# Optimization experiments

Hardware: AMD Instinct MI355X
Metric: run time of the kernel (lower is better)

## Reference

```python
import jax, jax.numpy as jnp
import numpy as np

DIM = 384
HEADS = 6
N_TOKEN = 2240
HIDDEN = int(DIM * 4.0)
EPS = 1e-5


def layernorm(x, g, b):
    mu = jnp.mean(x, axis=-1, keepdims=True)
    var = jnp.mean(jnp.square(x - mu), axis=-1, keepdims=True)
    return (x - mu) * jax.lax.rsqrt(var + EPS) * g + b


def setup_inputs() -> dict:
    key = jax.random.key(0)
    ks = jax.random.split(key, 10)
    B, N, C = 2, 2240, DIM
    s = 0.02
    return {
        "x": jax.random.normal(ks[0], (B, N, C), dtype=jnp.float32),
        "encoder_pos": jax.random.normal(ks[1], (1, N_TOKEN, C), dtype=jnp.float32) * s,
        "ln1_g": jnp.ones((C,), jnp.float32),
        "ln1_b": jnp.zeros((C,), jnp.float32),
        "w_qkv": jax.random.normal(ks[2], (3 * C, C), dtype=jnp.float32) * s,  # torch Linear [out,in], no bias
        "w_proj": jax.random.normal(ks[3], (C, C), dtype=jnp.float32) * s,
        "b_proj": jnp.zeros((C,), jnp.float32),
        "ln2_g": jnp.ones((C,), jnp.float32),
        "ln2_b": jnp.zeros((C,), jnp.float32),
        "w_fc1": jax.random.normal(ks[4], (HIDDEN, C), dtype=jnp.float32) * s,
        "b_fc1": jnp.zeros((HIDDEN,), jnp.float32),
        "w_fc2": jax.random.normal(ks[5], (C, HIDDEN), dtype=jnp.float32) * s,
        "b_fc2": jnp.zeros((C,), jnp.float32),
    }


def reference(x, encoder_pos, ln1_g, ln1_b, w_qkv, w_proj, b_proj, ln2_g, ln2_b, w_fc1, b_fc1, w_fc2, b_fc2):
    B, N, C = x.shape
    H = HEADS
    hd = C // H
    scale = hd ** -0.5

    # positional embedding: each of the n_token rows repeated N//n_token times (contiguously)
    rep = N // encoder_pos.shape[1]
    pos = jnp.repeat(encoder_pos, rep, axis=1)  # [1, N, C]
    x = x + pos

    # attention
    h = layernorm(x, ln1_g, ln1_b)
    qkv = h @ w_qkv.T  # [B, N, 3C]
    qkv = qkv.reshape(B, N, 3, H, hd).transpose(2, 0, 3, 1, 4)  # [3, B, H, N, hd]
    q, k, v = qkv[0], qkv[1], qkv[2]
    attn = jax.nn.softmax(jnp.einsum("bhqd,bhkd->bhqk", q, k) * scale, axis=-1)  # [B, H, N, N]
    o = jnp.einsum("bhqk,bhkd->bhqd", attn, v).transpose(0, 2, 1, 3).reshape(B, N, C)
    o = o @ w_proj.T + b_proj
    x = x + o

    # MLP
    h = layernorm(x, ln2_g, ln2_b)
    h = jax.nn.gelu(h @ w_fc1.T + b_fc1, approximate=False)
    h = h @ w_fc2.T + b_fc2
    x = x + h
    return (x, attn)
```

## Files before the change

### kernel.cpp

```cpp
#include <hip/hip_runtime.h>
#include <math.h>

typedef unsigned short u16;
typedef unsigned int   u32;
typedef __attribute__((ext_vector_type(8))) short short8;
typedef __attribute__((ext_vector_type(4))) float floatx4;

#define MFMA16(a,b,c) __builtin_amdgcn_mfma_f32_16x16x32_bf16((a),(b),(c),0,0,0)

constexpr int BB  = 2;
constexpr int NT  = 2240;
constexpr int CD  = 384;
constexpr int NH  = 6;
constexpr int HD  = 64;
constexpr int HID = 1536;
constexpr int M   = BB * NT;
constexpr int CS  = 5;
constexpr int CTILES = NT / 64 / CS;
constexpr float SCALE = 0.125f;

__device__ inline u16 f2bf(float f) {
  u32 u = __float_as_uint(f);
  u = (u + 0x7fffu + ((u >> 16) & 1u)) >> 16;
  return (u16)u;
}
__device__ inline float bf2f(u16 b) { return __uint_as_float(((u32)b) << 16); }

__device__ inline void gload16(const u16* g, u16* l) {
  __builtin_amdgcn_global_load_lds(
      (const __attribute__((address_space(1))) u32*)g,
      (__attribute__((address_space(3))) u32*)l, 16, 0, 0);
}

__device__ inline uint4 sum5_bf(uint4 a0, uint4 a1, uint4 a2, uint4 a3, uint4 a4) {
  union U { uint4 v; u16 h[8]; };
  U u0, u1, u2, u3, u4, o;
  u0.v = a0; u1.v = a1; u2.v = a2; u3.v = a3; u4.v = a4;
  #pragma unroll
  for (int e = 0; e < 8; ++e) {
    float f = bf2f(u0.h[e]) + bf2f(u1.h[e]) + bf2f(u2.h[e]) + bf2f(u3.h[e]) + bf2f(u4.h[e]);
    o.h[e] = f2bf(f);
  }
  return o.v;
}

constexpr int NQ = 3 * CD * CD, NP = CD * CD, N1 = HID * CD, N2 = CD * HID;
constexpr int CVT_BLOCKS = (NQ + NP + N1 + N2) / 512;

__global__ __launch_bounds__(128) void ln_cvt_kernel(
    const float* __restrict__ xin, const float* __restrict__ pos,
    const float* __restrict__ g, const float* __restrict__ bta,
    float* __restrict__ x1out, u16* __restrict__ hout,
    const float* __restrict__ s0, u16* __restrict__ d0,
    const float* __restrict__ s1, u16* __restrict__ d1,
    const float* __restrict__ s2, u16* __restrict__ d2,
    const float* __restrict__ s3, u16* __restrict__ d3) {
  int t = threadIdx.x;
  if (blockIdx.x >= M) {
    int i = ((blockIdx.x - M) * 128 + t) * 4;
    const float* s; u16* d; int base;
    if (i < NQ)                { s = s0; d = d0; base = 0; }
    else if (i < NQ + NP)      { s = s1; d = d1; base = NQ; }
    else if (i < NQ + NP + N1) { s = s2; d = d2; base = NQ + NP; }
    else                       { s = s3; d = d3; base = NQ + NP + N1; }
    int j = i - base;
    float4 v = *(const float4*)(s + j);
    ushort4 o; o.x = f2bf(v.x); o.y = f2bf(v.y); o.z = f2bf(v.z); o.w = f2bf(v.w);
    *(ushort4*)(d + j) = o;
    return;
  }
  int row = blockIdx.x;
  int n = row % NT;
  const float* xr = xin + (size_t)row * CD;
  float v[3], s1v = 0.f, s2v = 0.f;
  #pragma unroll
  for (int j = 0; j < 3; ++j) {
    int c = t + j * 128;
    float x = xr[c] + pos[(size_t)n * CD + c];
    v[j] = x; s1v += x; s2v += x * x;
  }
  #pragma unroll
  for (int off = 32; off; off >>= 1) { s1v += __shfl_down(s1v, off); s2v += __shfl_down(s2v, off); }
  __shared__ float rbuf[4];
  __shared__ float stats[2];
  int lane = t & 63, wid = t >> 6;
  if (lane == 0) { rbuf[wid] = s1v; rbuf[2 + wid] = s2v; }
  __syncthreads();
  if (t == 0) {
    float a = rbuf[0] + rbuf[1], b2 = rbuf[2] + rbuf[3];
    float mu = a / CD;
    float var = b2 / CD - mu * mu;
    stats[0] = mu; stats[1] = rsqrtf(var + 1e-5f);
  }
  __syncthreads();
  float mu = stats[0], rs = stats[1];
  #pragma unroll
  for (int j = 0; j < 3; ++j) {
    int c = t + j * 128;
    float h = (v[j] - mu) * rs * g[c] + bta[c];
    hout[(size_t)row * CD + c] = f2bf(h);
    x1out[(size_t)row * CD + c] = v[j];
  }
}

template <int EPI, int AMODE>
__global__ __launch_bounds__(256) void gemm_bt(
    const u16* __restrict__ A, const float* __restrict__ Af,
    const u16* __restrict__ Wt, int K,
    const float* __restrict__ bias, const float* __restrict__ res,
    const float* __restrict__ lng, const float* __restrict__ lnb,
    float* __restrict__ outf, u16* __restrict__ outb,
    u16* __restrict__ qout, u16* __restrict__ kout, u16* __restrict__ vtout) {
  __shared__ __align__(16) u16 As[64][64];
  __shared__ __align__(16) u16 Bs[64][64];
  __shared__ float mu_s[64], rs_s[64];
  int m0 = blockIdx.y * 64, n0 = blockIdx.x * 64;
  int t = threadIdx.x;
  int lane = t & 63, w = t >> 6, wm = w & 1, wn = w >> 1;
  int quad = lane >> 4, c16 = lane & 15;
  int lrow = t >> 2, lseg = t & 3;
  int l8 = lane >> 3;
  int colsel = ((lane & 7) ^ l8) * 8;
  int r7 = c16 & 7;

  const u16* gbsrc = Wt + (size_t)(n0 + w * 16 + l8) * K + colsel;
  u16* ldsB = &Bs[w * 16][0];
  const u16* gasrc = nullptr; u16* ldsA = nullptr;
  if constexpr (AMODE == 0) {
    gasrc = A + (size_t)(m0 + w * 16 + l8) * K + colsel;
    ldsA = &As[w * 16][0];
  }

  if constexpr (AMODE == 2) {
    const float* xr = Af + (size_t)(m0 + lrow) * CD + lseg * 96;
    float s1 = 0.f, s2 = 0.f;
    #pragma unroll
    for (int j2 = 0; j2 < 24; ++j2) {
      float4 v = *(const float4*)(xr + j2 * 4);
      s1 += v.x + v.y + v.z + v.w;
      s2 += v.x * v.x + v.y * v.y + v.z * v.z + v.w * v.w;
    }
    s1 += __shfl_xor(s1, 1); s2 += __shfl_xor(s2, 1);
    s1 += __shfl_xor(s1, 2); s2 += __shfl_xor(s2, 2);
    if (lseg == 0) {
      float mu = s1 / CD, var = s2 / CD - mu * mu;
      mu_s[lrow] = mu; rs_s[lrow] = rsqrtf(var + 1e-5f);
    }
  }

  constexpr int SL = (AMODE == 1) ? 5 : 1;
  const u16* ga[SL];
  uint4 av0[SL], av1[SL];
  float4 lf0, lf1, lf2, lf3;
  if constexpr (AMODE == 1) {
    #pragma unroll
    for (int s = 0; s < SL; ++s) {
      ga[s] = A + (size_t)s * M * CD + (size_t)(m0 + lrow) * CD + lseg * 8;
      av0[s] = *(const uint4*)(ga[s]);
      av1[s] = *(const uint4*)(ga[s] + 32);
    }
  } else if constexpr (AMODE == 2) {
    const float* ar = Af + (size_t)(m0 + lrow) * CD + lseg * 8;
    lf0 = *(const float4*)(ar);      lf1 = *(const float4*)(ar + 4);
    lf2 = *(const float4*)(ar + 32); lf3 = *(const float4*)(ar + 36);
  }

  floatx4 acc[2][2] = {};
  for (int k0 = 0; k0 < K; k0 += 64) {
    __syncthreads();
    #pragma unroll
    for (int j = 0; j < 2; ++j) {
      gload16(gbsrc + (size_t)j * 8 * K + k0, ldsB + j * 512);
      if constexpr (AMODE == 0)
        gload16(gasrc + (size_t)j * 8 * K + k0, ldsA + j * 512);
    }
    if constexpr (AMODE == 1) {
      uint4 wa0 = sum5_bf(av0[0], av0[1], av0[2], av0[3], av0[4]);
      uint4 wa1 = sum5_bf(av1[0], av1[1], av1[2], av1[3], av1[4]);
      *(uint4*)&As[lrow][(lseg ^ (lrow & 7)) * 8] = wa0;
      *(uint4*)&As[lrow][((4 + lseg) ^ (lrow & 7)) * 8] = wa1;
    } else if constexpr (AMODE == 2) {
      float mu = mu_s[lrow], rs = rs_s[lrow];
      union { uint4 v; u16 h[8]; } pk;
      int cb = k0 + lseg * 8;
      float4 g0 = *(const float4*)(lng + cb), g1 = *(const float4*)(lng + cb + 4);
      float4 b0 = *(const float4*)(lnb + cb), b1 = *(const float4*)(lnb + cb + 4);
      pk.h[0] = f2bf((lf0.x - mu) * rs * g0.x + b0.x);
      pk.h[1] = f2bf((lf0.y - mu) * rs * g0.y + b0.y);
      pk.h[2] = f2bf((lf0.z - mu) * rs * g0.z + b0.z);
      pk.h[3] = f2bf((lf0.w - mu) * rs * g0.w + b0.w);
      pk.h[4] = f2bf((lf1.x - mu) * rs * g1.x + b1.x);
      pk.h[5] = f2bf((lf1.y - mu) * rs * g1.y + b1.y);
      pk.h[6] = f2bf((lf1.z - mu) * rs * g1.z + b1.z);
      pk.h[7] = f2bf((lf1.w - mu) * rs * g1.w + b1.w);
      *(uint4*)&As[lrow][(lseg ^ (lrow & 7)) * 8] = pk.v;
      int cb2 = cb + 32;
      float4 g2 = *(const float4*)(lng + cb2), g3 = *(const float4*)(lng + cb2 + 4);
      float4 b2 = *(const float4*)(lnb + cb2), b3 = *(const float4*)(lnb + cb2 + 4);
      pk.h[0] = f2bf((lf2.x - mu) * rs * g2.x + b2.x);
      pk.h[1] = f2bf((lf2.y - mu) * rs * g2.y + b2.y);
      pk.h[2] = f2bf((lf2.z - mu) * rs * g2.z + b2.z);
      pk.h[3] = f2bf((lf2.w - mu) * rs * g2.w + b2.w);
      pk.h[4] = f2bf((lf3.x - mu) * rs * g3.x + b3.x);
      pk.h[5] = f2bf((lf3.y - mu) * rs * g3.y + b3.y);
      pk.h[6] = f2bf((lf3.z - mu) * rs * g3.z + b3.z);
      pk.h[7] = f2bf((lf3.w - mu) * rs * g3.w + b3.w);
      *(uint4*)&As[lrow][((4 + lseg) ^ (lrow & 7)) * 8] = pk.v;
    }
    __syncthreads();
    if (k0 + 64 < K) {
      if constexpr (AMODE == 1) {
        #pragma unroll
        for (int s = 0; s < SL; ++s) {
          av0[s] = *(const uint4*)(ga[s] + k0 + 64);
          av1[s] = *(const uint4*)(ga[s] + k0 + 96);
        }
      } else if constexpr (AMODE == 2) {
        const float* ar = Af + (size_t)(m0 + lrow) * CD + k0 + 64 + lseg * 8;
        lf0 = *(const float4*)(ar);      lf1 = *(const float4*)(ar + 4);
        lf2 = *(const float4*)(ar + 32); lf3 = *(const float4*)(ar + 36);
      }
    }
    #pragma unroll
    for (int ks = 0; ks < 2; ++ks) {
      int cswz = ((ks * 4 + quad) ^ r7) * 8;
      short8 af[2], bf[2];
      #pragma unroll
      for (int mt = 0; mt < 2; ++mt) af[mt] = *(const short8*)&As[wm * 32 + mt * 16 + c16][cswz];
      #pragma unroll
      for (int nt = 0; nt < 2; ++nt) bf[nt] = *(const short8*)&Bs[wn * 32 + nt * 16 + c16][cswz];
      #pragma unroll
      for (int mt = 0; mt < 2; ++mt)
        #pragma unroll
        for (int nt = 0; nt < 2; ++nt)
          acc[mt][nt] = MFMA16(af[mt], bf[nt], acc[mt][nt]);
    }
  }
  if constexpr (EPI == 0) {
    int s = n0 / 384;
    int hh = (n0 % 384) / 64;
    int b_ = m0 / NT, nn0 = m0 % NT;
    __syncthreads();
    #pragma unroll
    for (int mt = 0; mt < 2; ++mt)
      #pragma unroll
      for (int nt = 0; nt < 2; ++nt)
        #pragma unroll
        for (int r = 0; r < 4; ++r) {
          int m_l = wm * 32 + mt * 16 + quad * 4 + r;
          int d_l = wn * 32 + nt * 16 + c16;
          u16 bv = f2bf(acc[mt][nt][r]);
          if (s < 2) As[m_l][d_l ^ ((m_l & 7) << 3)] = bv;
          else       As[d_l][m_l ^ ((d_l & 7) << 3)] = bv;
        }
    __syncthreads();
    int row = t >> 2, q2 = (t & 3) * 2;
    uint4 va = *(const uint4*)&As[row][(q2 ^ (row & 7)) * 8];
    uint4 vb = *(const uint4*)&As[row][((q2 + 1) ^ (row & 7)) * 8];
    int cs0 = (t & 3) * 16;
    u16* dst;
    if (s == 0)      dst = qout  + ((size_t)(b_ * NH + hh) * NT + nn0 + row) * HD + cs0;
    else if (s == 1) dst = kout  + ((size_t)(b_ * NH + hh) * NT + nn0 + row) * HD + cs0;
    else             dst = vtout + ((size_t)(b_ * NH + hh) * HD + row) * NT + nn0 + cs0;
    *(uint4*)dst = va;
    *(uint4*)(dst + 8) = vb;
  } else {
    #pragma unroll
    for (int mt = 0; mt < 2; ++mt) {
      #pragma unroll
      for (int nt = 0; nt < 2; ++nt) {
        int rg0 = m0 + wm * 32 + mt * 16 + quad * 4;
        int cg = n0 + wn * 32 + nt * 16 + c16;
        #pragma unroll
        for (int r = 0; r < 4; ++r) {
          float v = acc[mt][nt][r];
          int m = rg0 + r;
          if constexpr (EPI == 2) {
            v += bias[cg];
            v = 0.5f * v * (1.0f + erff(v * 0.70710678118f));
            outb[(size_t)m * HID + cg] = f2bf(v);
          } else {
            outf[(size_t)m * CD + cg] = v + bias[cg] + res[(size_t)m * CD + cg];
          }
        }
      }
    }
  }
}

__global__ __launch_bounds__(256) void attn_pass1(
    const u16* __restrict__ qb, const u16* __restrict__ kb, float* __restrict__ ml) {
  __shared__ __align__(16) u16 Ks[64][72];
  int bh = blockIdx.y, chunk = blockIdx.z;
  int q0 = blockIdx.x * 64;
  int t = threadIdx.x, w = t >> 6, lane = t & 63, quad = lane >> 4, c16 = lane & 15;
  int lrow = t >> 2, lseg = t & 3;

  const u16* qp = qb + ((size_t)bh * NT + q0 + w * 16 + c16) * HD;
  short8 qf0 = *(const short8*)(qp + quad * 8);
  short8 qf1 = *(const short8*)(qp + 32 + quad * 8);
  const u16* kbase = kb + (size_t)bh * NT * HD;

  float m_i = -1e30f, l_i = 0.f;

  const u16* kg = kbase + (size_t)(chunk * CTILES * 64 + lrow) * HD + lseg * 8;
  uint4 kv0 = *(const uint4*)kg;
  uint4 kv1 = *(const uint4*)(kg + 32);

  for (int ct = 0; ct < CTILES; ++ct) {
    __syncthreads();
    *(uint4*)&Ks[lrow][lseg * 8] = kv0;
    *(uint4*)&Ks[lrow][32 + lseg * 8] = kv1;
    __syncthreads();
    if (ct + 1 < CTILES) {
      const u16* kn = kbase + (size_t)((chunk * CTILES + ct + 1) * 64 + lrow) * HD + lseg * 8;
      kv0 = *(const uint4*)kn;
      kv1 = *(const uint4*)(kn + 32);
    }
    floatx4 s_acc[4] = {};
    #pragma unroll
    for (int nt = 0; nt < 4; ++nt) {
      const u16* kp = &Ks[nt * 16 + c16][quad * 8];
      s_acc[nt] = MFMA16(*(const short8*)(kp), qf0, s_acc[nt]);
      s_acc[nt] = MFMA16(*(const short8*)(kp + 32), qf1, s_acc[nt]);
    }
    float rm = -1e30f;
    #pragma unroll
    for (int nt = 0; nt < 4; ++nt)
      #pragma unroll
      for (int r = 0; r < 4; ++r) rm = fmaxf(rm, s_acc[nt][r]);
    rm *= SCALE;
    rm = fmaxf(rm, __shfl_xor(rm, 16));
    rm = fmaxf(rm, __shfl_xor(rm, 32));
    float nm = fmaxf(m_i, rm);
    float ps = 0.f;
    #pragma unroll
    for (int nt = 0; nt < 4; ++nt)
      #pragma unroll
      for (int r = 0; r < 4; ++r) ps += __expf(s_acc[nt][r] * SCALE - nm);
    ps += __shfl_xor(ps, 16);
    ps += __shfl_xor(ps, 32);
    l_i = l_i * __expf(m_i - nm) + ps;
    m_i = nm;
  }
  if (quad == 0) {
    int row = q0 + w * 16 + c16;
    float* p = ml + ((size_t)(bh * NT + row) * CS + chunk) * 2;
    p[0] = m_i; p[1] = l_i;
  }
}

__global__ __launch_bounds__(256) void attn_pass2(
    const u16* __restrict__ qb, const u16* __restrict__ kb, const u16* __restrict__ vtb,
    const float* __restrict__ ml, float* __restrict__ attn_out, u16* __restrict__ o_part) {
  __shared__ __align__(16) u16 Ks[64][72];
  __shared__ __align__(16) u16 Vs[64][72];
  __shared__ __align__(16) u16 Plds[4][16][72];
  __shared__ float mfin[64], rlfin[64];
  int bh = blockIdx.y, chunk = blockIdx.z;
  int b = bh / NH, hh = bh % NH;
  int q0 = blockIdx.x * 64;
  int t = threadIdx.x, w = t >> 6, lane = t & 63, quad = lane >> 4, c16 = lane & 15;
  int lrow = t >> 2, lseg = t & 3;

  const u16* kbase = kb + (size_t)bh * NT * HD;
  const u16* vbase = vtb + (size_t)bh * HD * NT;

  int col00 = chunk * CTILES * 64;
  const u16* kg = kbase + (size_t)(col00 + lrow) * HD + lseg * 8;
  const u16* vg = vbase + (size_t)lrow * NT + col00 + lseg * 8;
  uint4 kv0 = *(const uint4*)kg;
  uint4 kv1 = *(const uint4*)(kg + 32);
  uint4 vv0 = *(const uint4*)vg;
  uint4 vv1 = *(const uint4*)(vg + 32);

  if (t < 64) {
    const float* p = ml + (size_t)(bh * NT + q0 + t) * CS * 2;
    float mm = -1e30f;
    #pragma unroll
    for (int c = 0; c < CS; ++c) mm = fmaxf(mm, p[c * 2]);
    float ll = 0.f;
    #pragma unroll
    for (int c = 0; c < CS; ++c) ll += p[c * 2 + 1] * __expf(p[c * 2] - mm);
    mfin[t] = mm; rlfin[t] = 1.0f / ll;
  }
  __syncthreads();
  float m_i[4], rl[4];
  #pragma unroll
  for (int r = 0; r < 4; ++r) {
    int rr = w * 16 + quad * 4 + r;
    m_i[r] = mfin[rr]; rl[r] = rlfin[rr];
  }

  const u16* qp = qb + ((size_t)bh * NT + q0 + w * 16 + c16) * HD;
  short8 qf0 = *(const short8*)(qp + quad * 8);
  short8 qf1 = *(const short8*)(qp + 32 + quad * 8);

  floatx4 o_acc[4] = {};
  float* attn_bh = attn_out + (size_t)bh * NT * NT;
  for (int ct = 0; ct < CTILES; ++ct) {
    int col0 = (chunk * CTILES + ct) * 64;
    __syncthreads();
    *(uint4*)&Ks[lrow][lseg * 8] = kv0;
    *(uint4*)&Ks[lrow][32 + lseg * 8] = kv1;
    *(uint4*)&Vs[lrow][lseg * 8] = vv0;
    *(uint4*)&Vs[lrow][32 + lseg * 8] = vv1;
    __syncthreads();
    if (ct + 1 < CTILES) {
      int coln = col0 + 64;
      const u16* kn = kbase + (size_t)(coln + lrow) * HD + lseg * 8;
      const u16* vn = vbase + (size_t)lrow * NT + coln + lseg * 8;
      kv0 = *(const uint4*)kn;
      kv1 = *(const uint4*)(kn + 32);
      vv0 = *(const uint4*)vn;
      vv1 = *(const uint4*)(vn + 32);
    }
    floatx4 s_acc[4] = {};
    #pragma unroll
    for (int nt = 0; nt < 4; ++nt) {
      const u16* kp = &Ks[nt * 16 + c16][quad * 8];
      s_acc[nt] = MFMA16(qf0, *(const short8*)(kp), s_acc[nt]);
      s_acc[nt] = MFMA16(qf1, *(const short8*)(kp + 32), s_acc[nt]);
    }
    #pragma unroll
    for (int nt = 0; nt < 4; ++nt) {
      #pragma unroll
      for (int r = 0; r < 4; ++r) {
        float p = __expf(s_acc[nt][r] * SCALE - m_i[r]) * rl[r];
        __builtin_nontemporal_store(
            p, &attn_bh[(size_t)(q0 + w * 16 + quad * 4 + r) * NT + col0 + nt * 16 + c16]);
        Plds[w][quad * 4 + r][nt * 16 + c16] = f2bf(p);
      }
    }
    #pragma unroll
    for (int ks = 0; ks < 2; ++ks) {
      short8 pa = *(const short8*)&Plds[w][c16][ks * 32 + quad * 8];
      #pragma unroll
      for (int dt = 0; dt < 4; ++dt) {
        short8 vb = *(const short8*)&Vs[dt * 16 + c16][ks * 32 + quad * 8];
        o_acc[dt] = MFMA16(pa, vb, o_acc[dt]);
      }
    }
  }
  #pragma unroll
  for (int dt = 0; dt < 4; ++dt) {
    #pragma unroll
    for (int r = 0; r < 4; ++r) {
      int m = b * NT + q0 + w * 16 + quad * 4 + r;
      int cc = hh * 64 + dt * 16 + c16;
      o_part[((size_t)chunk * M + m) * CD + cc] = f2bf(o_acc[dt][r]);
    }
  }
}

extern "C" void kernel_launch(void* const* d_in, const int* in_sizes, int n_in,
                              void* d_out, int out_size, void* d_ws, size_t ws_size,
                              hipStream_t stream) {
  const float* x      = (const float*)d_in[0];
  const float* pos    = (const float*)d_in[1];
  const float* ln1_g  = (const float*)d_in[2];
  const float* ln1_b  = (const float*)d_in[3];
  const float* w_qkv  = (const float*)d_in[4];
  const float* w_proj = (const float*)d_in[5];
  const float* b_proj = (const float*)d_in[6];
  const float* ln2_g  = (const float*)d_in[7];
  const float* ln2_b  = (const float*)d_in[8];
  const float* w_fc1  = (const float*)d_in[9];
  const float* b_fc1  = (const float*)d_in[10];
  const float* w_fc2  = (const float*)d_in[11];
  const float* b_fc2  = (const float*)d_in[12];

  float* out      = (float*)d_out;
  float* attn_out = out + (size_t)M * CD;

  char* ws = (char*)d_ws;
  size_t o = 0;
  auto carve = [&](size_t bytes) { char* p = ws + o; o += bytes; return p; };
  float* x1    = (float*)carve((size_t)M * CD * 4);
  u16* h1      = (u16*)carve((size_t)M * CD * 2);
  u16* wqkv_b  = (u16*)carve((size_t)3 * CD * CD * 2);
  u16* wproj_b = (u16*)carve((size_t)CD * CD * 2);
  u16* wfc1_b  = (u16*)carve((size_t)HID * CD * 2);
  u16* wfc2_b  = (u16*)carve((size_t)CD * HID * 2);
  u16* q_bf    = (u16*)carve((size_t)BB * NH * NT * HD * 2);
  u16* k_bf    = (u16*)carve((size_t)BB * NH * NT * HD * 2);
  u16* vt_bf   = (u16*)carve((size_t)BB * NH * NT * HD * 2);
  float* x2    = (float*)carve((size_t)M * CD * 4);
  u16* g_bf    = (u16*)carve((size_t)M * HID * 2);
  float* ml    = (float*)carve((size_t)NH * BB * NT * CS * 2 * 4);
  u16* o_part  = (u16*)carve((size_t)CS * M * CD * 2);
  (void)ws_size; (void)in_sizes; (void)n_in; (void)out_size;

  ln_cvt_kernel<<<M + CVT_BLOCKS, 128, 0, stream>>>(
      x, pos, ln1_g, ln1_b, x1, h1,
      w_qkv, wqkv_b, w_proj, wproj_b, w_fc1, wfc1_b, w_fc2, wfc2_b);

  gemm_bt<0, 0><<<dim3((3 * CD) / 64, M / 64), 256, 0, stream>>>(
      h1, nullptr, wqkv_b, CD, nullptr, nullptr, nullptr, nullptr,
      nullptr, nullptr, q_bf, k_bf, vt_bf);

  attn_pass1<<<dim3(NT / 64, BB * NH, CS), 256, 0, stream>>>(q_bf, k_bf, ml);
  attn_pass2<<<dim3(NT / 64, BB * NH, CS), 256, 0, stream>>>(q_bf, k_bf, vt_bf, ml, attn_out, o_part);

  gemm_bt<3, 1><<<dim3(CD / 64, M / 64), 256, 0, stream>>>(
      o_part, nullptr, wproj_b, CD, b_proj, x1, nullptr, nullptr,
      x2, nullptr, nullptr, nullptr, nullptr);

  gemm_bt<2, 2><<<dim3(HID / 64, M / 64), 256, 0, stream>>>(
      nullptr, x2, wfc1_b, CD, b_fc1, nullptr, ln2_g, ln2_b,
      nullptr, g_bf, nullptr, nullptr, nullptr);

  gemm_bt<3, 0><<<dim3(CD / 64, M / 64), 256, 0, stream>>>(
      g_bf, nullptr, wfc2_b, HID, b_fc2, x2, nullptr, nullptr,
      out, nullptr, nullptr, nullptr, nullptr);
}
```

Before: 432.8 us.

## Replace direct global-to-LDS loads with register-staged prefetch and padded LDS tiles

```diff
diff --git a/kernel.cpp b/kernel.cpp
--- a/kernel.cpp
+++ b/kernel.cpp
@@ -25,12 +25,6 @@
   return (u16)u;
 }
 __device__ inline float bf2f(u16 b) { return __uint_as_float(((u32)b) << 16); }
-
-__device__ inline void gload16(const u16* g, u16* l) {
-  __builtin_amdgcn_global_load_lds(
-      (const __attribute__((address_space(1))) u32*)g,
-      (__attribute__((address_space(3))) u32*)l, 16, 0, 0);
-}
 
 __device__ inline uint4 sum5_bf(uint4 a0, uint4 a1, uint4 a2, uint4 a3, uint4 a4) {
   union U { uint4 v; u16 h[8]; };
@@ -111,25 +105,14 @@
     const float* __restrict__ lng, const float* __restrict__ lnb,
     float* __restrict__ outf, u16* __restrict__ outb,
     u16* __restrict__ qout, u16* __restrict__ kout, u16* __restrict__ vtout) {
-  __shared__ __align__(16) u16 As[64][64];
-  __shared__ __align__(16) u16 Bs[64][64];
+  __shared__ __align__(16) u16 As[64][72];
+  __shared__ __align__(16) u16 Bs[64][72];
   __shared__ float mu_s[64], rs_s[64];
   int m0 = blockIdx.y * 64, n0 = blockIdx.x * 64;
   int t = threadIdx.x;
   int lane = t & 63, w = t >> 6, wm = w & 1, wn = w >> 1;
   int quad = lane >> 4, c16 = lane & 15;
   int lrow = t >> 2, lseg = t & 3;
-  int l8 = lane >> 3;
-  int colsel = ((lane & 7) ^ l8) * 8;
-  int r7 = c16 & 7;
-
-  const u16* gbsrc = Wt + (size_t)(n0 + w * 16 + l8) * K + colsel;
-  u16* ldsB = &Bs[w * 16][0];
-  const u16* gasrc = nullptr; u16* ldsA = nullptr;
-  if constexpr (AMODE == 0) {
-    gasrc = A + (size_t)(m0 + w * 16 + l8) * K + colsel;
-    ldsA = &As[w * 16][0];
-  }
 
   if constexpr (AMODE == 2) {
     const float* xr = Af + (size_t)(m0 + lrow) * CD + lseg * 96;
@@ -155,7 +138,7 @@
   if constexpr (AMODE == 1) {
     #pragma unroll
     for (int s = 0; s < SL; ++s) {
-      ga[s] = A + (size_t)s * M * CD + (size_t)(m0 + lrow) * CD + lseg * 8;
+      ga[s] = A + (size_t)s * M * CD + (size_t)(m0 + lrow) * K + lseg * 8;
       av0[s] = *(const uint4*)(ga[s]);
       av1[s] = *(const uint4*)(ga[s] + 32);
     }
@@ -163,22 +146,23 @@
     const float* ar = Af + (size_t)(m0 + lrow) * CD + lseg * 8;
     lf0 = *(const float4*)(ar);      lf1 = *(const float4*)(ar + 4);
     lf2 = *(const float4*)(ar + 32); lf3 = *(const float4*)(ar + 36);
-  }
+  } else {
+    ga[0] = A + (size_t)(m0 + lrow) * K + lseg * 8;
+    av0[0] = *(const uint4*)(ga[0]);
+    av1[0] = *(const uint4*)(ga[0] + 32);
+  }
+  const u16* gb = Wt + (size_t)(n0 + lrow) * K + lseg * 8;
+  uint4 bv0 = *(const uint4*)(gb);
+  uint4 bv1 = *(const uint4*)(gb + 32);
 
   floatx4 acc[2][2] = {};
   for (int k0 = 0; k0 < K; k0 += 64) {
     __syncthreads();
-    #pragma unroll
-    for (int j = 0; j < 2; ++j) {
-      gload16(gbsrc + (size_t)j * 8 * K + k0, ldsB + j * 512);
-      if constexpr (AMODE == 0)
-        gload16(gasrc + (size_t)j * 8 * K + k0, ldsA + j * 512);
-    }
     if constexpr (AMODE == 1) {
       uint4 wa0 = sum5_bf(av0[0], av0[1], av0[2], av0[3], av0[4]);
       uint4 wa1 = sum5_bf(av1[0], av1[1], av1[2], av1[3], av1[4]);
-      *(uint4*)&As[lrow][(lseg ^ (lrow & 7)) * 8] = wa0;
-      *(uint4*)&As[lrow][((4 + lseg) ^ (lrow & 7)) * 8] = wa1;
+      *(uint4*)&As[lrow][lseg * 8] = wa0;
+      *(uint4*)&As[lrow][32 + lseg * 8] = wa1;
     } else if constexpr (AMODE == 2) {
       float mu = mu_s[lrow], rs = rs_s[lrow];
       union { uint4 v; u16 h[8]; } pk;
@@ -193,7 +177,7 @@
       pk.h[5] = f2bf((lf1.y - mu) * rs * g1.y + b1.y);
       pk.h[6] = f2bf((lf1.z - mu) * rs * g1.z + b1.z);
       pk.h[7] = f2bf((lf1.w - mu) * rs * g1.w + b1.w);
-      *(uint4*)&As[lrow][(lseg ^ (lrow & 7)) * 8] = pk.v;
+      *(uint4*)&As[lrow][lseg * 8] = pk.v;
       int cb2 = cb + 32;
       float4 g2 = *(const float4*)(lng + cb2), g3 = *(const float4*)(lng + cb2 + 4);
       float4 b2 = *(const float4*)(lnb + cb2), b3 = *(const float4*)(lnb + cb2 + 4);
@@ -205,8 +189,13 @@
       pk.h[5] = f2bf((lf3.y - mu) * rs * g3.y + b3.y);
       pk.h[6] = f2bf((lf3.z - mu) * rs * g3.z + b3.z);
       pk.h[7] = f2bf((lf3.w - mu) * rs * g3.w + b3.w);
-      *(uint4*)&As[lrow][((4 + lseg) ^ (lrow & 7)) * 8] = pk.v;
-    }
+      *(uint4*)&As[lrow][32 + lseg * 8] = pk.v;
+    } else {
+      *(uint4*)&As[lrow][lseg * 8] = av0[0];
+      *(uint4*)&As[lrow][32 + lseg * 8] = av1[0];
+    }
+    *(uint4*)&Bs[lrow][lseg * 8] = bv0;
+    *(uint4*)&Bs[lrow][32 + lseg * 8] = bv1;
     __syncthreads();
     if (k0 + 64 < K) {
       if constexpr (AMODE == 1) {
@@ -219,16 +208,20 @@
         const float* ar = Af + (size_t)(m0 + lrow) * CD + k0 + 64 + lseg * 8;
         lf0 = *(const float4*)(ar);      lf1 = *(const float4*)(ar + 4);
         lf2 = *(const float4*)(ar + 32); lf3 = *(const float4*)(ar + 36);
+      } else {
+        av0[0] = *(const uint4*)(ga[0] + k0 + 64);
+        av1[0] = *(const uint4*)(ga[0] + k0 + 96);
       }
+      bv0 = *(const uint4*)(gb + k0 + 64);
+      bv1 = *(const uint4*)(gb + k0 + 96);
     }
     #pragma unroll
     for (int ks = 0; ks < 2; ++ks) {
-      int cswz = ((ks * 4 + quad) ^ r7) * 8;
       short8 af[2], bf[2];
       #pragma unroll
-      for (int mt = 0; mt < 2; ++mt) af[mt] = *(const short8*)&As[wm * 32 + mt * 16 + c16][cswz];
-      #pragma unroll
-      for (int nt = 0; nt < 2; ++nt) bf[nt] = *(const short8*)&Bs[wn * 32 + nt * 16 + c16][cswz];
+      for (int mt = 0; mt < 2; ++mt) af[mt] = *(const short8*)&As[wm * 32 + mt * 16 + c16][ks * 32 + quad * 8];
+      #pragma unroll
+      for (int nt = 0; nt < 2; ++nt) bf[nt] = *(const short8*)&Bs[wn * 32 + nt * 16 + c16][ks * 32 + quad * 8];
       #pragma unroll
       for (int mt = 0; mt < 2; ++mt)
         #pragma unroll
@@ -250,14 +243,13 @@
           int m_l = wm * 32 + mt * 16 + quad * 4 + r;
           int d_l = wn * 32 + nt * 16 + c16;
           u16 bv = f2bf(acc[mt][nt][r]);
-          if (s < 2) As[m_l][d_l ^ ((m_l & 7) << 3)] = bv;
-          else       As[d_l][m_l ^ ((d_l & 7) << 3)] = bv;
+          if (s < 2) As[m_l][d_l] = bv;
+          else       As[d_l][m_l] = bv;
         }
     __syncthreads();
-    int row = t >> 2, q2 = (t & 3) * 2;
-    uint4 va = *(const uint4*)&As[row][(q2 ^ (row & 7)) * 8];
-    uint4 vb = *(const uint4*)&As[row][((q2 + 1) ^ (row & 7)) * 8];
-    int cs0 = (t & 3) * 16;
+    int row = t >> 2, cs0 = (t & 3) * 16;
+    uint4 va = *(const uint4*)&As[row][cs0];
+    uint4 vb = *(const uint4*)&As[row][cs0 + 8];
     u16* dst;
     if (s == 0)      dst = qout  + ((size_t)(b_ * NH + hh) * NT + nn0 + row) * HD + cs0;
     else if (s == 1) dst = kout  + ((size_t)(b_ * NH + hh) * NT + nn0 + row) * HD + cs0;
```

New measurement: 431.6 us. No clear change (-0.3%).
